# Performance work log

Hardware: AMD Instinct MI355X
Metric: run time of the kernel (lower is better)

## Reference

```python
import jax, jax.numpy as jnp
import numpy as np

WEIGHT_BIT = 8
BIAS_BIT = 32
EPS = 1e-8


def setup_inputs() -> dict:
    key = jax.random.key(0)
    k1, k2, k3, k4 = jax.random.split(key, 4)
    N, IN, OUT = 65536, 512, 512
    # x_q: already-quantized int8-range activations stored as float32
    x_q = jax.random.randint(k1, (N, IN), -128, 128).astype(jnp.float32)
    weight = jax.random.normal(k2, (OUT, IN), dtype=jnp.float32) * 0.05
    bias = jax.random.normal(k3, (OUT,), dtype=jnp.float32) * 0.01
    scale_x = jax.random.uniform(k4, (1,), dtype=jnp.float32, minval=0.01, maxval=0.1)
    return {"x_q": x_q, "weight": weight, "bias": bias, "scale_x": scale_x}


def _symmetric_quant_weight(w, bit):
    # per-output-channel symmetric quantization (min/max over dim=1)
    n = float(2 ** (bit - 1) - 1)  # 127 for 8-bit
    sat = jnp.maximum(jnp.abs(w.min(axis=1)), jnp.abs(w.max(axis=1)))  # [OUT]
    scale = jnp.maximum(sat, EPS) / n                                   # [OUT]
    w_q = jnp.clip(jnp.round(w / scale[:, None]), -n - 1.0, n)
    return w_q, scale


def reference(x_q, weight, bias, scale_x):
    w_q, scale_w = _symmetric_quant_weight(weight, WEIGHT_BIT)
    scale_out = scale_w * scale_x[0]          # [OUT] per-channel output scale
    nb = float(2 ** (BIAS_BIT - 1) - 1)
    b_q = jnp.clip(jnp.round(bias / scale_out), -nb - 1.0, nb)
    # integer-only matmul: int32 GEMM with int32 bias
    out_q = (jnp.dot(x_q.astype(jnp.int32), w_q.astype(jnp.int32).T)
             + b_q.astype(jnp.int32)[None, :])
    return out_q, scale_out.reshape(1, -1)
```

## Files before the change

kernel.cpp:

```cpp
#include <hip/hip_runtime.h>
#include <hip/hip_bf16.h>

typedef __attribute__((ext_vector_type(8))) short bf16x8;
typedef __attribute__((ext_vector_type(4))) float f32x4;

#define KDIM 512
#define NDIM 512
#define BM 128
#define BN 128
#define BK 64
#define NT (KDIM / BK)

__device__ __forceinline__ unsigned int pack_bf16(float a, float b) {
  return (__builtin_bit_cast(unsigned int, a) >> 16) |
         (__builtin_bit_cast(unsigned int, b) & 0xffff0000u);
}

__global__ __launch_bounds__(64)
void quant_w_kernel(const float* __restrict__ W, const float* __restrict__ bias,
                    const float* __restrict__ scale_x,
                    ushort* __restrict__ Wq, float* __restrict__ bq,
                    float* __restrict__ so_out) {
  const int n = blockIdx.x;
  const int l = threadIdx.x;
  const float* row = W + (size_t)n * KDIM;
  float4 v0 = *(const float4*)(row + l * 8);
  float4 v1 = *(const float4*)(row + l * 8 + 4);
  float m = fmaxf(fmaxf(fmaxf(fabsf(v0.x), fabsf(v0.y)), fmaxf(fabsf(v0.z), fabsf(v0.w))),
                  fmaxf(fmaxf(fabsf(v1.x), fabsf(v1.y)), fmaxf(fabsf(v1.z), fabsf(v1.w))));
#pragma unroll
  for (int off = 32; off; off >>= 1) m = fmaxf(m, __shfl_xor(m, off, 64));
  const float scale = fmaxf(m, 1e-8f) / 127.0f;
  float vals[8] = {v0.x, v0.y, v0.z, v0.w, v1.x, v1.y, v1.z, v1.w};
  unsigned int packed[4];
#pragma unroll
  for (int i = 0; i < 4; ++i) {
    float qa = fminf(fmaxf(rintf(vals[2 * i] / scale), -128.f), 127.f);
    float qb = fminf(fmaxf(rintf(vals[2 * i + 1] / scale), -128.f), 127.f);
    packed[i] = pack_bf16(qa, qb);
  }
  *(uint4*)(Wq + (size_t)n * KDIM + (size_t)l * 8) =
      make_uint4(packed[0], packed[1], packed[2], packed[3]);
  if (l == 0) {
    float so = scale * scale_x[0];
    so_out[n] = so;
    bq[n] = rintf(bias[n] / so);
  }
}

__global__ __launch_bounds__(256, 2)
void gemm_kernel(const float* __restrict__ X, const ushort* __restrict__ Wq,
                 const float* __restrict__ bq, float* __restrict__ Out) {
  __shared__ __align__(16) ushort As[2][BM * BK];
  __shared__ __align__(16) ushort Bs[2][BN * BK];

  const int nblk = gridDim.x;
  int swz = blockIdx.x;
  if ((nblk & 7) == 0) {
    swz = (blockIdx.x & 7) * (nblk >> 3) + (blockIdx.x >> 3);
  }
  const int bm = swz >> 2;
  const int bn = swz & 3;

  const int tid = threadIdx.x;
  const int l = tid & 63, w = tid >> 6;
  const int wr = w >> 1, wc = w & 1;
  const int lr = l & 15, lk = l >> 4;

  const float* xbase = X + (size_t)bm * BM * KDIM;
  const ushort* wbase = Wq + (size_t)bn * BN * KDIM;

  float4 av[8];
  f32x4 acc[4][4];
#pragma unroll
  for (int i = 0; i < 4; ++i)
#pragma unroll
    for (int j = 0; j < 4; ++j) acc[i][j] = (f32x4){0.f, 0.f, 0.f, 0.f};

  auto loadA = [&](int t) {
#pragma unroll
    for (int i = 0; i < 8; ++i) {
      int e = i * 256 + tid;
      int row = e >> 4, c4 = e & 15;
      av[i] = *(const float4*)(xbase + (size_t)row * KDIM + t * BK + c4 * 4);
    }
  };
  auto writeA = [&](int buf) {
    char* sA = (char*)&As[buf][0];
#pragma unroll
    for (int i = 0; i < 8; ++i) {
      int e = i * 256 + tid;
      int row = e >> 4, c4 = e & 15;
      int byteo = (row * 128 + c4 * 8) ^ ((row & 7) << 4);
      uint2 p;
      p.x = pack_bf16(av[i].x, av[i].y);
      p.y = pack_bf16(av[i].z, av[i].w);
      *(uint2*)(sA + byteo) = p;
    }
  };
  auto stageB = [&](int t, int buf) {
#pragma unroll
    for (int i = 0; i < 4; ++i) {
      int c = w * 4 + i;
      int s = c * 64 + l;
      int row = s >> 3, kc = s & 7;
      int skc = kc ^ (row & 7);
      const ushort* g = wbase + (size_t)row * KDIM + t * BK + skc * 8;
      ushort* lp = &Bs[buf][0] + (size_t)s * 8;
      __builtin_amdgcn_global_load_lds(
          (const __attribute__((address_space(1))) unsigned int*)g,
          (__attribute__((address_space(3))) unsigned int*)lp, 16, 0, 0);
    }
  };
  auto compute = [&](int buf) {
    const char* pA = (const char*)&As[buf][0];
    const char* pB = (const char*)&Bs[buf][0];
#pragma unroll
    for (int ks = 0; ks < 2; ++ks) {
      bf16x8 af[4], bfr[4];
#pragma unroll
      for (int mf = 0; mf < 4; ++mf) {
        int row = wr * 64 + mf * 16 + lr;
        int byteo = (row * 128 + (ks * 4 + lk) * 16) ^ ((row & 7) << 4);
        af[mf] = *(const bf16x8*)(pA + byteo);
      }
#pragma unroll
      for (int nf = 0; nf < 4; ++nf) {
        int row = wc * 64 + nf * 16 + lr;
        int byteo = (row * 128 + (ks * 4 + lk) * 16) ^ ((row & 7) << 4);
        bfr[nf] = *(const bf16x8*)(pB + byteo);
      }
#pragma unroll
      for (int mf = 0; mf < 4; ++mf)
#pragma unroll
        for (int nf = 0; nf < 4; ++nf)
          acc[mf][nf] = __builtin_amdgcn_mfma_f32_16x16x32_bf16(
              af[mf], bfr[nf], acc[mf][nf], 0, 0, 0);
    }
  };

  stageB(0, 0);
  loadA(0);
  writeA(0);
  __syncthreads();

  int cur = 0;
  for (int t = 0; t < NT; ++t) {
    if (t < NT - 1) {
      stageB(t + 1, cur ^ 1);
      loadA(t + 1);
    }
    compute(cur);
    if (t < NT - 1) writeA(cur ^ 1);
    __syncthreads();
    cur ^= 1;
  }

  const size_t m0 = (size_t)bm * BM + (size_t)wr * 64;
  const int n0 = bn * BN + wc * 64;
#pragma unroll
  for (int nf = 0; nf < 4; ++nf) {
    const int col = n0 + nf * 16 + lr;
    const float bqv = bq[col];
#pragma unroll
    for (int mf = 0; mf < 4; ++mf) {
      const size_t rbase = m0 + (size_t)mf * 16 + (size_t)lk * 4;
#pragma unroll
      for (int e = 0; e < 4; ++e)
        Out[(rbase + e) * NDIM + col] = acc[mf][nf][e] + bqv;
    }
  }
}

extern "C" void kernel_launch(void* const* d_in, const int* in_sizes, int n_in,
                              void* d_out, int out_size, void* d_ws, size_t ws_size,
                              hipStream_t stream) {
  const float* x = (const float*)d_in[0];
  const float* weight = (const float*)d_in[1];
  const float* bias = (const float*)d_in[2];
  const float* scale_x = (const float*)d_in[3];
  const int M = in_sizes[0] / KDIM;

  float* out = (float*)d_out;
  float* so_out = out + (size_t)M * NDIM;
  ushort* Wq = (ushort*)d_ws;
  float* bq = (float*)((char*)d_ws + (size_t)NDIM * KDIM * sizeof(ushort));

  quant_w_kernel<<<NDIM, 64, 0, stream>>>(weight, bias, scale_x, Wq, bq, so_out);

  const int blocks = (M / BM) * (NDIM / BN);
  gemm_kernel<<<blocks, 256, 0, stream>>>(x, Wq, bq, out);
}
```

Before: 281.4 us.

## Pre-swizzle quantized weights into MFMA fragment layout and read B from global

The weight quantization kernel now writes Wq in a fragment-major layout, so each GEMM lane can load its B operand directly from global/L2 with one 16-byte load, with no LDS staging. Each wave owns a private 32x128 output tile and its own double-buffered A region in LDS. This removes block-wide __syncthreads and cuts LDS use, allowing three blocks per CU. The output goes through an LDS transpose so each row is written with wide vector stores. The cost is that every wave re-reads all 128 columns of B from cache and A reuse across waves is lost.

Result: slower. 346.7 us (+23.2%).

```diff
diff --git a/kernel.cpp b/kernel.cpp
--- a/kernel.cpp
+++ b/kernel.cpp
@@ -8,6 +8,7 @@
 #define NDIM 512
 #define BM 128
 #define BN 128
+#define WROWS 32
 #define BK 64
 #define NT (KDIM / BK)
 
@@ -19,7 +20,7 @@
 __global__ __launch_bounds__(64)
 void quant_w_kernel(const float* __restrict__ W, const float* __restrict__ bias,
                     const float* __restrict__ scale_x,
-                    ushort* __restrict__ Wq, float* __restrict__ bq,
+                    ushort* __restrict__ Wq_arr, float* __restrict__ bq,
                     float* __restrict__ so_out) {
   const int n = blockIdx.x;
   const int l = threadIdx.x;
@@ -39,8 +40,8 @@
     float qb = fminf(fmaxf(rintf(vals[2 * i + 1] / scale), -128.f), 127.f);
     packed[i] = pack_bf16(qa, qb);
   }
-  *(uint4*)(Wq + (size_t)n * KDIM + (size_t)l * 8) =
-      make_uint4(packed[0], packed[1], packed[2], packed[3]);
+  const size_t slot = ((size_t)(n >> 4) * 16 + (l >> 2)) * 64 + (n & 15) + (l & 3) * 16;
+  *(uint4*)(Wq_arr + slot * 8) = make_uint4(packed[0], packed[1], packed[2], packed[3]);
   if (l == 0) {
     float so = scale * scale_x[0];
     so_out[n] = so;
@@ -48,126 +49,107 @@
   }
 }
 
-__global__ __launch_bounds__(256, 2)
-void gemm_kernel(const float* __restrict__ X, const ushort* __restrict__ Wq,
+__global__ __launch_bounds__(256, 3)
+void gemm_kernel(const float* __restrict__ X, const ushort* __restrict__ Wqa,
                  const float* __restrict__ bq, float* __restrict__ Out) {
-  __shared__ __align__(16) ushort As[2][BM * BK];
-  __shared__ __align__(16) ushort Bs[2][BN * BK];
+  __shared__ __align__(16) char smem[4][8192];
 
   const int nblk = gridDim.x;
   int swz = blockIdx.x;
-  if ((nblk & 7) == 0) {
+  if ((nblk & 7) == 0)
     swz = (blockIdx.x & 7) * (nblk >> 3) + (blockIdx.x >> 3);
-  }
   const int bm = swz >> 2;
   const int bn = swz & 3;
 
   const int tid = threadIdx.x;
   const int l = tid & 63, w = tid >> 6;
-  const int wr = w >> 1, wc = w & 1;
   const int lr = l & 15, lk = l >> 4;
 
-  const float* xbase = X + (size_t)bm * BM * KDIM;
-  const ushort* wbase = Wq + (size_t)bn * BN * KDIM;
+  const int wrow0 = bm * BM + w * WROWS;
+  const float* xbase = X + (size_t)wrow0 * KDIM;
+  char* sA = smem[w];
 
-  float4 av[8];
-  f32x4 acc[4][4];
+  f32x4 acc[2][8];
 #pragma unroll
-  for (int i = 0; i < 4; ++i)
+  for (int i = 0; i < 2; ++i)
 #pragma unroll
-    for (int j = 0; j < 4; ++j) acc[i][j] = (f32x4){0.f, 0.f, 0.f, 0.f};
+    for (int j = 0; j < 8; ++j) acc[i][j] = (f32x4){0.f, 0.f, 0.f, 0.f};
 
-  auto loadA = [&](int t) {
+  float4 raw[8];
+  auto gloadA = [&](int t) {
+#pragma unroll
+    for (int i = 0; i < 8; ++i)
+      raw[i] = *(const float4*)(xbase + (size_t)(i * 4 + lk) * KDIM + t * BK + lr * 4);
+  };
+  auto packwrite = [&](char* buf) {
 #pragma unroll
     for (int i = 0; i < 8; ++i) {
-      int e = i * 256 + tid;
-      int row = e >> 4, c4 = e & 15;
-      av[i] = *(const float4*)(xbase + (size_t)row * KDIM + t * BK + c4 * 4);
+      int lrow = i * 4 + lk;
+      int byteo = (lrow * 128 + lr * 8) ^ ((lrow & 7) << 4);
+      uint2 p;
+      p.x = pack_bf16(raw[i].x, raw[i].y);
+      p.y = pack_bf16(raw[i].z, raw[i].w);
+      *(uint2*)(buf + byteo) = p;
     }
   };
-  auto writeA = [&](int buf) {
-    char* sA = (char*)&As[buf][0];
+  auto readA = [&](const char* buf, int mf, int ks) -> bf16x8 {
+    int lrow = mf * 16 + lr;
+    int byteo = (lrow * 128 + (ks * 4 + lk) * 16) ^ ((lrow & 7) << 4);
+    return *(const bf16x8*)(buf + byteo);
+  };
+
+  gloadA(0);
+  packwrite(sA);
+  gloadA(1);
+
+  for (int t = 0; t < NT; ++t) {
+    char* bufc = sA + (t & 1) * 4096;
+    char* bufn = sA + ((t + 1) & 1) * 4096;
+    bf16x8 af[2][2];
 #pragma unroll
-    for (int i = 0; i < 8; ++i) {
-      int e = i * 256 + tid;
-      int row = e >> 4, c4 = e & 15;
-      int byteo = (row * 128 + c4 * 8) ^ ((row & 7) << 4);
-      uint2 p;
-      p.x = pack_bf16(av[i].x, av[i].y);
-      p.y = pack_bf16(av[i].z, av[i].w);
-      *(uint2*)(sA + byteo) = p;
-    }
-  };
-  auto stageB = [&](int t, int buf) {
+    for (int mf = 0; mf < 2; ++mf)
 #pragma unroll
-    for (int i = 0; i < 4; ++i) {
-      int c = w * 4 + i;
-      int s = c * 64 + l;
-      int row = s >> 3, kc = s & 7;
-      int skc = kc ^ (row & 7);
-      const ushort* g = wbase + (size_t)row * KDIM + t * BK + skc * 8;
-      ushort* lp = &Bs[buf][0] + (size_t)s * 8;
-      __builtin_amdgcn_global_load_lds(
-          (const __attribute__((address_space(1))) unsigned int*)g,
-          (__attribute__((address_space(3))) unsigned int*)lp, 16, 0, 0);
-    }
-  };
-  auto compute = [&](int buf) {
-    const char* pA = (const char*)&As[buf][0];
-    const char* pB = (const char*)&Bs[buf][0];
+      for (int ks = 0; ks < 2; ++ks) af[mf][ks] = readA(bufc, mf, ks);
+    if (t < NT - 1) packwrite(bufn);
 #pragma unroll
     for (int ks = 0; ks < 2; ++ks) {
-      bf16x8 af[4], bfr[4];
+      const int kt = t * 2 + ks;
+      bf16x8 bf[8];
 #pragma unroll
-      for (int mf = 0; mf < 4; ++mf) {
-        int row = wr * 64 + mf * 16 + lr;
-        int byteo = (row * 128 + (ks * 4 + lk) * 16) ^ ((row & 7) << 4);
-        af[mf] = *(const bf16x8*)(pA + byteo);
-      }
+      for (int nf = 0; nf < 8; ++nf)
+        bf[nf] = *(const bf16x8*)(Wqa + (((size_t)(bn * 8 + nf) * 16 + kt) * 64 + l) * 8);
 #pragma unroll
-      for (int nf = 0; nf < 4; ++nf) {
-        int row = wc * 64 + nf * 16 + lr;
-        int byteo = (row * 128 + (ks * 4 + lk) * 16) ^ ((row & 7) << 4);
-        bfr[nf] = *(const bf16x8*)(pB + byteo);
-      }
+      for (int mf = 0; mf < 2; ++mf)
 #pragma unroll
-      for (int mf = 0; mf < 4; ++mf)
-#pragma unroll
-        for (int nf = 0; nf < 4; ++nf)
-          acc[mf][nf] = __builtin_amdgcn_mfma_f32_16x16x32_bf16(
-              af[mf], bfr[nf], acc[mf][nf], 0, 0, 0);
+        for (int nf = 0; nf < 8; ++nf)
+          acc[mf][nf] = __builtin_amdgcn_mfma_f32_16x16x32_bf16(af[mf][ks], bf[nf],
+                                                                acc[mf][nf], 0, 0, 0);
     }
-  };
-
-  stageB(0, 0);
-  loadA(0);
-  writeA(0);
-  __syncthreads();
-
-  int cur = 0;
-  for (int t = 0; t < NT; ++t) {
-    if (t < NT - 1) {
-      stageB(t + 1, cur ^ 1);
-      loadA(t + 1);
-    }
-    compute(cur);
-    if (t < NT - 1) writeA(cur ^ 1);
-    __syncthreads();
-    cur ^= 1;
+    if (t < NT - 2) gloadA(t + 2);
   }
 
-  const size_t m0 = (size_t)bm * BM + (size_t)wr * 64;
-  const int n0 = bn * BN + wc * 64;
+  float bqv[8];
 #pragma unroll
-  for (int nf = 0; nf < 4; ++nf) {
-    const int col = n0 + nf * 16 + lr;
-    const float bqv = bq[col];
+  for (int nf = 0; nf < 8; ++nf) bqv[nf] = bq[bn * BN + nf * 16 + lr];
+
+  float* fs = (float*)sA;
 #pragma unroll
-    for (int mf = 0; mf < 4; ++mf) {
-      const size_t rbase = m0 + (size_t)mf * 16 + (size_t)lk * 4;
+  for (int mf = 0; mf < 2; ++mf) {
 #pragma unroll
-      for (int e = 0; e < 4; ++e)
-        Out[(rbase + e) * NDIM + col] = acc[mf][nf][e] + bqv;
+    for (int nf = 0; nf < 8; ++nf) {
+      const int col = nf * 16 + lr;
+#pragma unroll
+      for (int e = 0; e < 4; ++e) {
+        int r = lk * 4 + e;
+        fs[r * 128 + (col ^ ((r & 12) << 2))] = acc[mf][nf][e] + bqv[nf];
+      }
+    }
+#pragma unroll
+    for (int j = 0; j < 8; ++j) {
+      const int r = j * 2 + (l >> 5);
+      const int c4 = (l & 31) * 4;
+      f32x4 v = *(const f32x4*)(fs + r * 128 + (c4 ^ ((r & 12) << 2)));
+      *(f32x4*)(Out + (size_t)(wrow0 + mf * 16 + r) * NDIM + bn * BN + c4) = v;
     }
   }
 }
@@ -183,11 +165,11 @@
 
   float* out = (float*)d_out;
   float* so_out = out + (size_t)M * NDIM;
-  ushort* Wq = (ushort*)d_ws;
+  ushort* Wq_arr = (ushort*)d_ws;
   float* bq = (float*)((char*)d_ws + (size_t)NDIM * KDIM * sizeof(ushort));
 
-  quant_w_kernel<<<NDIM, 64, 0, stream>>>(weight, bias, scale_x, Wq, bq, so_out);
+  quant_w_kernel<<<NDIM, 64, 0, stream>>>(weight, bias, scale_x, Wq_arr, bq, so_out);
 
   const int blocks = (M / BM) * (NDIM / BN);
-  gemm_kernel<<<blocks, 256, 0, stream>>>(x, Wq, bq, out);
+  gemm_kernel<<<blocks, 256, 0, stream>>>(x, Wq_arr, bq, out);
 }
```
